# Kernel tuning notes

Hardware: AMD Instinct MI355X
Metric: run time of the kernel (lower is better)

## Reference

```python
import jax, jax.numpy as jnp
import numpy as np

N, E, D, H, C, G = 80000, 1280000, 64, 64, 5, 512


def setup_inputs() -> dict:
    key = jax.random.key(0)
    ks = jax.random.split(key, 8)
    h = jax.random.normal(ks[0], (N, D), jnp.float32)
    src = jax.random.randint(ks[1], (E,), 0, N)
    dst = jax.random.randint(ks[2], (E,), 0, N)
    graph_ids = jnp.sort(jax.random.randint(ks[3], (N,), 0, G))
    # Glorot-ish init for weights
    W1 = jax.random.normal(ks[4], (D, H), jnp.float32) * (1.0 / np.sqrt(D))
    b1 = jnp.zeros((H,), jnp.float32)
    W2 = jax.random.normal(ks[5], (H, H), jnp.float32) * (1.0 / np.sqrt(H))
    b2 = jnp.zeros((H,), jnp.float32)
    Wc = jax.random.normal(ks[6], (H, C), jnp.float32) * (1.0 / np.sqrt(H))
    bc = jnp.zeros((C,), jnp.float32)
    return dict(h=h, src=src, dst=dst, graph_ids=graph_ids,
                W1=W1, b1=b1, W2=W2, b2=b2, Wc=Wc, bc=bc, num_graphs=G)


def reference(h, src, dst, graph_ids, W1, b1, W2, b2, Wc, bc, num_graphs):
    n = h.shape[0]
    ones_e = jnp.ones(src.shape[0], h.dtype)
    # DGL GraphConv norm='both': symmetric normalization, degrees clamped to >=1
    out_deg = jnp.clip(jax.ops.segment_sum(ones_e, src, num_segments=n), 1.0)
    in_deg = jnp.clip(jax.ops.segment_sum(ones_e, dst, num_segments=n), 1.0)
    norm_src = jax.lax.rsqrt(out_deg)  # [N]
    norm_dst = jax.lax.rsqrt(in_deg)   # [N]

    def graph_conv(x, W, b):
        x = x * norm_src[:, None]                                   # scale by D_out^{-1/2}
        agg = jax.ops.segment_sum(x[src], dst, num_segments=n)      # sparse A^T x (copy_u + sum)
        agg = agg * norm_dst[:, None]                               # scale by D_in^{-1/2}
        return agg @ W + b

    h1 = jax.nn.relu(graph_conv(h, W1, b1))
    h2 = jax.nn.relu(graph_conv(h1, W2, b2))

    # dgl.mean_nodes: per-graph mean pooling over nodes
    cnt = jnp.clip(jax.ops.segment_sum(jnp.ones(n, h.dtype), graph_ids,
                                       num_segments=num_graphs), 1.0)
    hg = jax.ops.segment_sum(h2, graph_ids, num_segments=num_graphs) / cnt[:, None]
    return hg @ Wc + bc  # [G, C] logits
```

## Files before the change

kernel.cpp:

```cpp
#include <hip/hip_runtime.h>
#include <hip/hip_bf16.h>


#define NBK 160
#define HB  256
#define CAP 9216

typedef __attribute__((ext_vector_type(8))) short bf16x8;
typedef __attribute__((ext_vector_type(4))) float f32x4;

__device__ __forceinline__ float bflo(unsigned u) { return __uint_as_float(u << 16); }
__device__ __forceinline__ float bfhi(unsigned u) { return __uint_as_float(u & 0xffff0000u); }
__device__ __forceinline__ float bf1(unsigned short u) { return __uint_as_float((unsigned)u << 16); }
__device__ __forceinline__ unsigned short f2bf(float f) {
    unsigned u = __float_as_uint(f);
    return (unsigned short)((u + 0x7fff + ((u >> 16) & 1)) >> 16);
}
__device__ __forceinline__ unsigned packbf(float lo, float hi) {
    return (unsigned)f2bf(lo) | ((unsigned)f2bf(hi) << 16);
}

__global__ __launch_bounds__(256) void pA_scatter(
    const int* __restrict__ src, const int* __restrict__ dst,
    int* __restrict__ curD, int* __restrict__ curS,
    int* __restrict__ pack, unsigned short* __restrict__ sloc,
    const int* __restrict__ gids, int* __restrict__ goffs,
    int E, int NB, int N, int G)
{
    if (blockIdx.x >= HB) {
        int i = (blockIdx.x - HB) * 256 + threadIdx.x;
        if (i >= N) return;
        int b = gids[i];
        if (i == 0) {
            for (int g = 0; g <= b; g++) goffs[g] = 0;
        } else {
            int a = gids[i - 1];
            for (int g = a + 1; g <= b; g++) goffs[g] = i;
        }
        if (i == N - 1) {
            for (int g = b + 1; g <= G; g++) goffs[g] = N;
        }
        return;
    }
    __shared__ int hd[NBK], hs[NBK];
    int t = threadIdx.x;
    for (int i = t; i < NB; i += 256) { hd[i] = 0; hs[i] = 0; }
    __syncthreads();
    int chunk = (E + HB - 1) / HB;
    int s0 = blockIdx.x * chunk, s1 = min(E, s0 + chunk);
    int q0 = s0 >> 2, q1 = s1 >> 2;
    const int4* s4 = (const int4*)src;
    const int4* d4 = (const int4*)dst;
    for (int q = q0 + t; q < q1; q += 256) {
        int4 d = d4[q];
        int4 s = s4[q];
        atomicAdd(&hd[d.x >> 9], 1); atomicAdd(&hd[d.y >> 9], 1);
        atomicAdd(&hd[d.z >> 9], 1); atomicAdd(&hd[d.w >> 9], 1);
        atomicAdd(&hs[s.x >> 9], 1); atomicAdd(&hs[s.y >> 9], 1);
        atomicAdd(&hs[s.z >> 9], 1); atomicAdd(&hs[s.w >> 9], 1);
    }
    for (int i = (q1 << 2) + t; i < s1; i += 256) {
        atomicAdd(&hd[dst[i] >> 9], 1);
        atomicAdd(&hs[src[i] >> 9], 1);
    }
    __syncthreads();
    for (int b = t; b < NB; b += 256) {
        int cd = hd[b], cs = hs[b];
        hd[b] = cd ? atomicAdd(&curD[b], cd) : 0;
        hs[b] = cs ? atomicAdd(&curS[b], cs) : 0;
    }
    __syncthreads();
    for (int q = q0 + t; q < q1; q += 256) {
        int4 d = d4[q];
        int4 s = s4[q];
        #pragma unroll
        for (int j = 0; j < 4; j++) {
            int ss = j == 0 ? s.x : j == 1 ? s.y : j == 2 ? s.z : s.w;
            int dd = j == 0 ? d.x : j == 1 ? d.y : j == 2 ? d.z : d.w;
            int bd = dd >> 9, bs = ss >> 9;
            int pd = atomicAdd(&hd[bd], 1);
            int ps = atomicAdd(&hs[bs], 1);
            if (pd < CAP) pack[(size_t)bd * CAP + pd] = ((dd & 511) << 17) | ss;
            if (ps < CAP) sloc[(size_t)bs * CAP + ps] = (unsigned short)(ss & 511);
        }
    }
    for (int i = (q1 << 2) + t; i < s1; i += 256) {
        int s = src[i], d = dst[i];
        int bd = d >> 9, bs = s >> 9;
        int pd = atomicAdd(&hd[bd], 1);
        int ps = atomicAdd(&hs[bs], 1);
        if (pd < CAP) pack[(size_t)bd * CAP + pd] = ((d & 511) << 17) | s;
        if (ps < CAP) sloc[(size_t)bs * CAP + ps] = (unsigned short)(s & 511);
    }
}

__global__ __launch_bounds__(256) void p5_build(
    const int* __restrict__ pack, const unsigned short* __restrict__ sloc,
    const int* __restrict__ curD, const int* __restrict__ curS,
    int* __restrict__ col, int* __restrict__ row_offs, int* __restrict__ deg,
    float* __restrict__ nsrc, float* __restrict__ ndst,
    const float* __restrict__ h, unsigned short* __restrict__ xs,
    int N, int NB)
{
    __shared__ int hist[512];
    __shared__ float nsl[512];
    __shared__ int wt[4];
    int t = threadIdx.x;
    bool dmode = blockIdx.x < NB;
    int b = dmode ? blockIdx.x : blockIdx.x - NB;
    int n0 = b << 9, n1 = min(N, n0 + 512);
    hist[t] = 0; hist[t + 256] = 0;
    __syncthreads();
    int e0 = b * CAP;
    int tot = min(dmode ? curD[b] : curS[b], CAP);
    int e1 = e0 + tot;
    if (!dmode) {
        for (int i = e0 + t; i < e1; i += 256)
            atomicAdd(&hist[sloc[i]], 1);
        __syncthreads();
        for (int n = n0 + t; n < n1; n += 256) {
            float s = rsqrtf((float)max(hist[n - n0], 1));
            nsrc[n] = s;
            nsl[n - n0] = s;
        }
        __syncthreads();
        int cnt = n1 - n0;
        const float2* h2p = (const float2*)h;
        ushort2* xp = (ushort2*)xs;
        for (int i = t; i < cnt * 32; i += 256) {
            int node = i >> 5;
            float s = nsl[node];
            float2 v = h2p[(size_t)(n0 + node) * 32 + (i & 31)];
            ushort2 o;
            o.x = f2bf(v.x * s);
            o.y = f2bf(v.y * s);
            xp[(size_t)(n0 + node) * 32 + (i & 31)] = o;
        }
        return;
    }
    for (int i = e0 + t; i < e1; i += 256)
        atomicAdd(&hist[pack[i] >> 17], 1);
    __syncthreads();
    int c0 = hist[2 * t], c1 = hist[2 * t + 1];
    int v = c0 + c1;
    int lane = t & 63, w = t >> 6;
    int x = v;
    #pragma unroll
    for (int off = 1; off < 64; off <<= 1) {
        int y = __shfl_up(x, off);
        if (lane >= off) x += y;
    }
    if (lane == 63) wt[w] = x;
    __syncthreads();
    int bw = 0;
    for (int i = 0; i < w; i++) bw += wt[i];
    int excl = x - v + bw;
    int n = n0 + 2 * t;
    if (n < n1) {
        row_offs[n] = e0 + excl;
        deg[n] = c0;
        ndst[n] = rsqrtf((float)max(c0, 1));
    }
    if (n + 1 < n1) {
        row_offs[n + 1] = e0 + excl + c0;
        deg[n + 1] = c1;
        ndst[n + 1] = rsqrtf((float)max(c1, 1));
    }
    hist[2 * t] = excl;
    hist[2 * t + 1] = excl + c0;
    __syncthreads();
    for (int i = e0 + t; i < e1; i += 256) {
        int wd = pack[i];
        int pos = atomicAdd(&hist[wd >> 17], 1);
        col[e0 + pos] = wd & 0x1FFFF;
    }
}

__global__ __launch_bounds__(256) void agg_kernel(
    const unsigned short* __restrict__ z, unsigned short* __restrict__ y,
    const int* __restrict__ col, const int* __restrict__ row_offs,
    const int* __restrict__ deg, int N)
{
    int lane = threadIdx.x & 63;
    int sub  = lane >> 3;
    int li   = lane & 7;
    const uint4* x4 = (const uint4*)z;

    int wid = (blockIdx.x * 256 + threadIdx.x) >> 6;
    int nw  = (gridDim.x * 256) >> 6;

    int ro = 0, cnt = 0, idx = 0;
    if (wid < N) {
        ro = row_offs[wid];
        cnt = deg[wid];
        if (lane < min(cnt, 64)) idx = col[ro + lane];
    }
    for (int node = wid; node < N; node += nw) {
        int nnode = node + nw;
        int nro = 0, ncnt = 0;
        if (nnode < N) { nro = row_offs[nnode]; ncnt = deg[nnode]; }

        float a0=0.f,a1=0.f,a2=0.f,a3=0.f,a4=0.f,a5=0.f,a6=0.f,a7=0.f;
        int cc = 0;
        int cidx = idx;
        while (cc < cnt) {
            int m = min(cnt - cc, 64);
            for (int i = 0; i < m; i += 32) {
                int e1 = i + sub, e2 = i + 8 + sub, e3 = i + 16 + sub, e4 = i + 24 + sub;
                int s1 = __shfl(cidx, min(e1, m - 1));
                int s2 = __shfl(cidx, min(e2, m - 1));
                int s3 = __shfl(cidx, min(e3, m - 1));
                int s4 = __shfl(cidx, min(e4, m - 1));
                uint4 v1 = make_uint4(0u,0u,0u,0u), v2 = v1, v3 = v1, v4 = v1;
                if (e1 < m) v1 = x4[(size_t)s1 * 8 + li];
                if (e2 < m) v2 = x4[(size_t)s2 * 8 + li];
                if (e3 < m) v3 = x4[(size_t)s3 * 8 + li];
                if (e4 < m) v4 = x4[(size_t)s4 * 8 + li];
                a0 += bflo(v1.x); a1 += bfhi(v1.x);
                a2 += bflo(v1.y); a3 += bfhi(v1.y);
                a4 += bflo(v1.z); a5 += bfhi(v1.z);
                a6 += bflo(v1.w); a7 += bfhi(v1.w);
                a0 += bflo(v2.x); a1 += bfhi(v2.x);
                a2 += bflo(v2.y); a3 += bfhi(v2.y);
                a4 += bflo(v2.z); a5 += bfhi(v2.z);
                a6 += bflo(v2.w); a7 += bfhi(v2.w);
                a0 += bflo(v3.x); a1 += bfhi(v3.x);
                a2 += bflo(v3.y); a3 += bfhi(v3.y);
                a4 += bflo(v3.z); a5 += bfhi(v3.z);
                a6 += bflo(v3.w); a7 += bfhi(v3.w);
                a0 += bflo(v4.x); a1 += bfhi(v4.x);
                a2 += bflo(v4.y); a3 += bfhi(v4.y);
                a4 += bflo(v4.z); a5 += bfhi(v4.z);
                a6 += bflo(v4.w); a7 += bfhi(v4.w);
            }
            cc += 64;
            if (cc < cnt) cidx = (lane < min(cnt - cc, 64)) ? col[ro + cc + lane] : 0;
        }
        idx = 0;
        if (nnode < N && lane < min(ncnt, 64)) idx = col[nro + lane];

        #pragma unroll
        for (int off = 8; off <= 32; off <<= 1) {
            a0 += __shfl_xor(a0, off); a1 += __shfl_xor(a1, off);
            a2 += __shfl_xor(a2, off); a3 += __shfl_xor(a3, off);
            a4 += __shfl_xor(a4, off); a5 += __shfl_xor(a5, off);
            a6 += __shfl_xor(a6, off); a7 += __shfl_xor(a7, off);
        }
        if (sub == 0) {
            uint4 o;
            o.x = packbf(a0, a1);
            o.y = packbf(a2, a3);
            o.z = packbf(a4, a5);
            o.w = packbf(a6, a7);
            ((uint4*)y)[(size_t)node * 8 + li] = o;
        }
        ro = nro; cnt = ncnt;
    }
}

__global__ __launch_bounds__(256) void gemm_kernel(
    const unsigned short* __restrict__ A, const float* __restrict__ W,
    const float* __restrict__ b, const float* __restrict__ ndst,
    const float* __restrict__ nsrc, unsigned short* __restrict__ Z,
    int M, int scale_out)
{
    int t = threadIdx.x, lane = t & 63, w = t >> 6;
    int col = lane & 15, quad = lane >> 4;
    bf16x8 bfrag[4][2];
    #pragma unroll
    for (int nt = 0; nt < 4; nt++)
        #pragma unroll
        for (int ks = 0; ks < 2; ks++)
            #pragma unroll
            for (int j = 0; j < 8; j++)
                bfrag[nt][ks][j] =
                    (short)f2bf(W[(ks * 32 + quad * 8 + j) * 64 + nt * 16 + col]);
    float bias[4];
    #pragma unroll
    for (int nt = 0; nt < 4; nt++) bias[nt] = b[nt * 16 + col];

    int mbase = blockIdx.x * 64 + w * 16;
    if (mbase >= M) return;
    int row = min(mbase + col, M - 1);
    const uint4* a4 = (const uint4*)A;
    union { uint4 u; bf16x8 v; } a0, a1;
    a0.u = a4[(size_t)row * 8 + quad];
    a1.u = a4[(size_t)row * 8 + 4 + quad];

    float nd[4], ns[4];
    #pragma unroll
    for (int r = 0; r < 4; r++) {
        int m = min(mbase + quad * 4 + r, M - 1);
        nd[r] = ndst[m];
        ns[r] = scale_out ? nsrc[m] : 1.f;
    }

    #pragma unroll
    for (int nt = 0; nt < 4; nt++) {
        f32x4 acc = {0.f, 0.f, 0.f, 0.f};
        acc = __builtin_amdgcn_mfma_f32_16x16x32_bf16(a0.v, bfrag[nt][0], acc, 0, 0, 0);
        acc = __builtin_amdgcn_mfma_f32_16x16x32_bf16(a1.v, bfrag[nt][1], acc, 0, 0, 0);
        #pragma unroll
        for (int r = 0; r < 4; r++) {
            int m = mbase + quad * 4 + r;
            if (m < M)
                Z[(size_t)m * 64 + nt * 16 + col] =
                    f2bf(fmaxf(nd[r] * acc[r] + bias[nt], 0.f) * ns[r]);
        }
    }
}

__global__ __launch_bounds__(256) void pool_kernel(
    const unsigned short* __restrict__ h2, const int* __restrict__ goffs,
    const float* __restrict__ Wc, const float* __restrict__ bc,
    float* __restrict__ out)
{
    int g = blockIdx.x;
    int lane = threadIdx.x & 63;
    int w = threadIdx.x >> 6;
    int s = goffs[g], e = goffs[g + 1];
    float acc = 0.f;
    for (int i = s + w; i < e; i += 4) acc += bf1(h2[i * 64 + lane]);
    __shared__ float red[4][64];
    red[w][lane] = acc;
    __syncthreads();
    if (w == 0) {
        float tot = red[0][lane] + red[1][lane] + red[2][lane] + red[3][lane];
        float mean = tot / (float)max(e - s, 1);
        float wc[5];
        #pragma unroll
        for (int c = 0; c < 5; c++) wc[c] = Wc[lane * 5 + c];
        #pragma unroll
        for (int c = 0; c < 5; c++) {
            float p = mean * wc[c];
            #pragma unroll
            for (int off = 32; off; off >>= 1) p += __shfl_down(p, off);
            if (lane == 0) out[g * 5 + c] = p + bc[c];
        }
    }
}

extern "C" void kernel_launch(void* const* d_in, const int* in_sizes, int n_in,
                              void* d_out, int out_size, void* d_ws, size_t ws_size,
                              hipStream_t stream)
{
    const float* h    = (const float*)d_in[0];
    const int*   src  = (const int*)d_in[1];
    const int*   dst  = (const int*)d_in[2];
    const int*   gids = (const int*)d_in[3];
    const float* W1   = (const float*)d_in[4];
    const float* b1   = (const float*)d_in[5];
    const float* W2   = (const float*)d_in[6];
    const float* b2   = (const float*)d_in[7];
    const float* Wc   = (const float*)d_in[8];
    const float* bc   = (const float*)d_in[9];
    float* out = (float*)d_out;

    const int N = in_sizes[0] / 64;
    const int E = in_sizes[1];
    const int G = out_size / 5;
    const int NB = (N + 511) >> 9;
    const int NBB = (N + 255) / 256;

    auto align = [](size_t x) { return (x + 255) & ~(size_t)255; };
    char* p = (char*)d_ws;
    int* curD    = (int*)p;            p += align((size_t)2 * NBK * 4);
    int* curS    = curD + NBK;
    int* row_offs= (int*)p;            p += align((size_t)N * 4);
    int* deg     = (int*)p;            p += align((size_t)N * 4);
    float* nsrc  = (float*)p;          p += align((size_t)N * 4);
    float* ndst  = (float*)p;          p += align((size_t)N * 4);
    int* goffs   = (int*)p;            p += align((size_t)(G + 1) * 4);
    int* pack    = (int*)p;            p += align((size_t)NBK * CAP * 4);
    unsigned short* sloc = (unsigned short*)p; p += align((size_t)NBK * CAP * 2);
    int* col     = (int*)p;            p += align((size_t)NBK * CAP * 4);
    unsigned short* xs  = (unsigned short*)p; p += align((size_t)N * 64 * 2);
    unsigned short* s1  = (unsigned short*)p; p += align((size_t)N * 64 * 2);
    unsigned short* h1s = (unsigned short*)p; p += align((size_t)N * 64 * 2);
    unsigned short* s2  = s1;
    unsigned short* h2  = xs;

    hipMemsetAsync(curD, 0, (size_t)2 * NBK * 4, stream);

    pA_scatter<<<HB + NBB, 256, 0, stream>>>(src, dst, curD, curS, pack, sloc,
                                             gids, goffs, E, NB, N, G);
    p5_build<<<2 * NB, 256, 0, stream>>>(pack, sloc, curD, curS, col,
                                         row_offs, deg, nsrc, ndst, h, xs, N, NB);

    agg_kernel<<<4096, 256, 0, stream>>>(xs, s1, col, row_offs, deg, N);
    gemm_kernel<<<(N + 63) / 64, 256, 0, stream>>>(s1, W1, b1, ndst, nsrc,
                                                   h1s, N, 1);
    agg_kernel<<<4096, 256, 0, stream>>>(h1s, s2, col, row_offs, deg, N);
    gemm_kernel<<<(N + 63) / 64, 256, 0, stream>>>(s2, W2, b2, ndst, nsrc,
                                                   h2, N, 0);

    pool_kernel<<<G, 256, 0, stream>>>(h2, goffs, Wc, bc, out);
}
```

Measured before the change: 223.9 us.

## Aggregate two consecutive nodes per wavefront in the gather kernel

Each wavefront now processes a pair of adjacent destination nodes, loading both nodes' neighbor indices in one coalesced read when their combined degree fits in 64. Gathers for both nodes are interleaved so more loads are in flight per iteration and the wave's index load serves two rows. This drops the previous software prefetch of the next node's row offsets and indices. It adds a second accumulator set, doubles the shuffle reductions, and falls back to a serial per-node loop for high-degree pairs.

New measurement: 234.2 us. +4.6%, slower.

```diff
diff --git a/kernel.cpp b/kernel.cpp
--- a/kernel.cpp
+++ b/kernel.cpp
@@ -189,72 +189,109 @@
     int wid = (blockIdx.x * 256 + threadIdx.x) >> 6;
     int nw  = (gridDim.x * 256) >> 6;
 
-    int ro = 0, cnt = 0, idx = 0;
-    if (wid < N) {
-        ro = row_offs[wid];
-        cnt = deg[wid];
-        if (lane < min(cnt, 64)) idx = col[ro + lane];
-    }
-    for (int node = wid; node < N; node += nw) {
-        int nnode = node + nw;
-        int nro = 0, ncnt = 0;
-        if (nnode < N) { nro = row_offs[nnode]; ncnt = deg[nnode]; }
-
-        float a0=0.f,a1=0.f,a2=0.f,a3=0.f,a4=0.f,a5=0.f,a6=0.f,a7=0.f;
-        int cc = 0;
-        int cidx = idx;
-        while (cc < cnt) {
-            int m = min(cnt - cc, 64);
-            for (int i = 0; i < m; i += 32) {
-                int e1 = i + sub, e2 = i + 8 + sub, e3 = i + 16 + sub, e4 = i + 24 + sub;
-                int s1 = __shfl(cidx, min(e1, m - 1));
-                int s2 = __shfl(cidx, min(e2, m - 1));
-                int s3 = __shfl(cidx, min(e3, m - 1));
-                int s4 = __shfl(cidx, min(e4, m - 1));
-                uint4 v1 = make_uint4(0u,0u,0u,0u), v2 = v1, v3 = v1, v4 = v1;
-                if (e1 < m) v1 = x4[(size_t)s1 * 8 + li];
-                if (e2 < m) v2 = x4[(size_t)s2 * 8 + li];
-                if (e3 < m) v3 = x4[(size_t)s3 * 8 + li];
-                if (e4 < m) v4 = x4[(size_t)s4 * 8 + li];
-                a0 += bflo(v1.x); a1 += bfhi(v1.x);
-                a2 += bflo(v1.y); a3 += bfhi(v1.y);
-                a4 += bflo(v1.z); a5 += bfhi(v1.z);
-                a6 += bflo(v1.w); a7 += bfhi(v1.w);
-                a0 += bflo(v2.x); a1 += bfhi(v2.x);
-                a2 += bflo(v2.y); a3 += bfhi(v2.y);
-                a4 += bflo(v2.z); a5 += bfhi(v2.z);
-                a6 += bflo(v2.w); a7 += bfhi(v2.w);
-                a0 += bflo(v3.x); a1 += bfhi(v3.x);
-                a2 += bflo(v3.y); a3 += bfhi(v3.y);
-                a4 += bflo(v3.z); a5 += bfhi(v3.z);
-                a6 += bflo(v3.w); a7 += bfhi(v3.w);
-                a0 += bflo(v4.x); a1 += bfhi(v4.x);
-                a2 += bflo(v4.y); a3 += bfhi(v4.y);
-                a4 += bflo(v4.z); a5 += bfhi(v4.z);
-                a6 += bflo(v4.w); a7 += bfhi(v4.w);
+    for (int pr = wid; 2 * pr < N; pr += nw) {
+        int n0 = 2 * pr, n1 = n0 + 1;
+        int ro0 = row_offs[n0];
+        int c0  = deg[n0];
+        int c1  = (n1 < N) ? deg[n1] : 0;
+        int ctot = c0 + c1;
+        float A[8], B[8];
+        #pragma unroll
+        for (int k = 0; k < 8; k++) { A[k] = 0.f; B[k] = 0.f; }
+
+        if (ctot <= 64) {
+            int idx = 0;
+            if (lane < ctot) idx = col[ro0 + lane];
+            int cm0 = max(c0 - 1, 0), cm1 = max(c1 - 1, 0);
+            int mx = max(c0, c1);
+            for (int i = 0; i < mx; i += 16) {
+                int e0 = i + sub, e1 = i + 8 + sub;
+                int s0 = __shfl(idx, min(e0, cm0));
+                int s1 = __shfl(idx, min(e1, cm0));
+                int t0 = __shfl(idx, c0 + min(e0, cm1));
+                int t1 = __shfl(idx, c0 + min(e1, cm1));
+                uint4 v0 = make_uint4(0u,0u,0u,0u), v1 = v0, w0 = v0, w1 = v0;
+                if (e0 < c0) v0 = x4[(size_t)s0 * 8 + li];
+                if (e1 < c0) v1 = x4[(size_t)s1 * 8 + li];
+                if (e0 < c1) w0 = x4[(size_t)t0 * 8 + li];
+                if (e1 < c1) w1 = x4[(size_t)t1 * 8 + li];
+                A[0] += bflo(v0.x); A[1] += bfhi(v0.x);
+                A[2] += bflo(v0.y); A[3] += bfhi(v0.y);
+                A[4] += bflo(v0.z); A[5] += bfhi(v0.z);
+                A[6] += bflo(v0.w); A[7] += bfhi(v0.w);
+                A[0] += bflo(v1.x); A[1] += bfhi(v1.x);
+                A[2] += bflo(v1.y); A[3] += bfhi(v1.y);
+                A[4] += bflo(v1.z); A[5] += bfhi(v1.z);
+                A[6] += bflo(v1.w); A[7] += bfhi(v1.w);
+                B[0] += bflo(w0.x); B[1] += bfhi(w0.x);
+                B[2] += bflo(w0.y); B[3] += bfhi(w0.y);
+                B[4] += bflo(w0.z); B[5] += bfhi(w0.z);
+                B[6] += bflo(w0.w); B[7] += bfhi(w0.w);
+                B[0] += bflo(w1.x); B[1] += bfhi(w1.x);
+                B[2] += bflo(w1.y); B[3] += bfhi(w1.y);
+                B[4] += bflo(w1.z); B[5] += bfhi(w1.z);
+                B[6] += bflo(w1.w); B[7] += bfhi(w1.w);
             }
-            cc += 64;
-            if (cc < cnt) cidx = (lane < min(cnt - cc, 64)) ? col[ro + cc + lane] : 0;
-        }
-        idx = 0;
-        if (nnode < N && lane < min(ncnt, 64)) idx = col[nro + lane];
+        } else {
+            #pragma unroll 1
+            for (int nn = 0; nn < 2; nn++) {
+                int cnt = nn ? c1 : c0;
+                int ro  = nn ? ro0 + c0 : ro0;
+                float T[8];
+                #pragma unroll
+                for (int k = 0; k < 8; k++) T[k] = 0.f;
+                int cc = 0;
+                while (cc < cnt) {
+                    int m = min(cnt - cc, 64);
+                    int cidx = (lane < m) ? col[ro + cc + lane] : 0;
+                    for (int i = 0; i < m; i += 16) {
+                        int e0 = i + sub, e1 = i + 8 + sub;
+                        int s0 = __shfl(cidx, min(e0, m - 1));
+                        int s1 = __shfl(cidx, min(e1, m - 1));
+                        uint4 v0 = make_uint4(0u,0u,0u,0u), v1 = v0;
+                        if (e0 < m) v0 = x4[(size_t)s0 * 8 + li];
+                        if (e1 < m) v1 = x4[(size_t)s1 * 8 + li];
+                        T[0] += bflo(v0.x); T[1] += bfhi(v0.x);
+                        T[2] += bflo(v0.y); T[3] += bfhi(v0.y);
+                        T[4] += bflo(v0.z); T[5] += bfhi(v0.z);
+                        T[6] += bflo(v0.w); T[7] += bfhi(v0.w);
+                        T[0] += bflo(v1.x); T[1] += bfhi(v1.x);
+                        T[2] += bflo(v1.y); T[3] += bfhi(v1.y);
+                        T[4] += bflo(v1.z); T[5] += bfhi(v1.z);
+                        T[6] += bflo(v1.w); T[7] += bfhi(v1.w);
+                    }
+                    cc += 64;
+                }
+                #pragma unroll
+                for (int k = 0; k < 8; k++) {
+                    if (nn == 0) A[k] = T[k]; else B[k] = T[k];
+                }
+            }
+        }
 
         #pragma unroll
         for (int off = 8; off <= 32; off <<= 1) {
-            a0 += __shfl_xor(a0, off); a1 += __shfl_xor(a1, off);
-            a2 += __shfl_xor(a2, off); a3 += __shfl_xor(a3, off);
-            a4 += __shfl_xor(a4, off); a5 += __shfl_xor(a5, off);
-            a6 += __shfl_xor(a6, off); a7 += __shfl_xor(a7, off);
+            #pragma unroll
+            for (int k = 0; k < 8; k++) {
+                A[k] += __shfl_xor(A[k], off);
+                B[k] += __shfl_xor(B[k], off);
+            }
         }
         if (sub == 0) {
             uint4 o;
-            o.x = packbf(a0, a1);
-            o.y = packbf(a2, a3);
-            o.z = packbf(a4, a5);
-            o.w = packbf(a6, a7);
-            ((uint4*)y)[(size_t)node * 8 + li] = o;
-        }
-        ro = nro; cnt = ncnt;
+            o.x = packbf(A[0], A[1]);
+            o.y = packbf(A[2], A[3]);
+            o.z = packbf(A[4], A[5]);
+            o.w = packbf(A[6], A[7]);
+            ((uint4*)y)[(size_t)n0 * 8 + li] = o;
+        } else if (sub == 1 && n1 < N) {
+            uint4 o;
+            o.x = packbf(B[0], B[1]);
+            o.y = packbf(B[2], B[3]);
+            o.z = packbf(B[4], B[5]);
+            o.w = packbf(B[6], B[7]);
+            ((uint4*)y)[(size_t)n1 * 8 + li] = o;
+        }
     }
 }
 
```
